# Performance work log

Hardware: AMD Instinct MI355X
Metric: run time of the kernel (lower is better)

The kernel has to match this reference:

```python
import jax, jax.numpy as jnp
import numpy as np

N_NODES = 100000
N_EDGES = 3200000
IN_DIM = 256
HID = 128
OUT = 2
BN_EPS = 1e-5


def setup_inputs() -> dict:
    key = jax.random.key(0)
    ks = jax.random.split(key, 4)
    x = jax.random.normal(ks[0], (N_NODES, IN_DIM), dtype=jnp.float32)
    edge_index = jax.random.randint(ks[1], (2, N_EDGES), 0, N_NODES, dtype=jnp.int64)
    # Glorot-ish scaled weights
    W1 = jax.random.normal(ks[2], (IN_DIM, HID), dtype=jnp.float32) * (1.0 / np.sqrt(IN_DIM))
    W2 = jax.random.normal(ks[3], (HID, OUT), dtype=jnp.float32) * (1.0 / np.sqrt(HID))
    return {
        "x": x,
        "edge_index": edge_index,
        "feature_importance": jnp.ones((IN_DIM,), jnp.float32),
        "W1": W1,
        "b1": jnp.zeros((HID,), jnp.float32),
        "W2": W2,
        "b2": jnp.zeros((OUT,), jnp.float32),
        "gamma": jnp.ones((HID,), jnp.float32),
        "beta": jnp.zeros((HID,), jnp.float32),
    }


def _gcn_conv(x, row, col, norm, W, b, n_nodes):
    # PyG GCNConv: linear transform then D^-1/2 (A+I) D^-1/2 aggregation
    h = x @ W  # [N, d_out]
    msg = h[row] * norm[:, None]  # gather + scale, [E+N, d_out]
    out = jax.ops.segment_sum(msg, col, num_segments=n_nodes)  # scatter-add
    return out + b


def _norm_and_loops(edge_index, n_nodes, dtype):
    loop = jnp.arange(n_nodes, dtype=edge_index.dtype)
    row = jnp.concatenate([edge_index[0], loop])
    col = jnp.concatenate([edge_index[1], loop])
    deg = jax.ops.segment_sum(jnp.ones_like(col, dtype=dtype), col, num_segments=n_nodes)
    dinv = jnp.where(deg > 0, jax.lax.rsqrt(deg), 0.0)
    norm = dinv[row] * dinv[col]
    return row, col, norm


def reference(x, edge_index, feature_importance, W1, b1, W2, b2, gamma, beta):
    n_nodes = x.shape[0]
    row, col, norm = _norm_and_loops(edge_index, n_nodes, x.dtype)
    # sigmoid feature-importance weighting
    xw = x * jax.nn.sigmoid(feature_importance)
    h = _gcn_conv(xw, row, col, norm, W1, b1, n_nodes)
    # BatchNorm1d with batch statistics (training-mode math; dropout omitted = eval)
    mu = jnp.mean(h, axis=0)
    var = jnp.mean((h - mu) ** 2, axis=0)
    h = (h - mu) * jax.lax.rsqrt(var + BN_EPS) * gamma + beta
    h = jax.nn.relu(h)
    out = _gcn_conv(h, row, col, norm, W2, b2, n_nodes)
    return out
```

## Files before the change

kernel.cpp:

```cpp
#include <hip/hip_runtime.h>
#include <hip/hip_bf16.h>

#define N_NODES 100000
#define N_EDGES 3200000
#define IN_DIM 256
#define HID 128
#define BN_EPS 1e-5f
#define SCAN_B 1024
#define NB1 ((N_NODES + SCAN_B - 1) / SCAN_B)

typedef __attribute__((ext_vector_type(8))) short bf16x8;
typedef __attribute__((ext_vector_type(4))) float f32x4;

__device__ __forceinline__ ushort f2bf(float f) {
    unsigned u = __float_as_uint(f);
    u += 0x7FFFu + ((u >> 16) & 1u);
    return (ushort)(u >> 16);
}
__device__ __forceinline__ float bflo(unsigned v) { return __uint_as_float(v << 16); }
__device__ __forceinline__ float bfhi(unsigned v) { return __uint_as_float(v & 0xFFFF0000u); }


__global__ void k_deg(const int* __restrict__ col, unsigned* __restrict__ cnt) {
    int i = blockIdx.x * blockDim.x + threadIdx.x;
    if (i < N_EDGES) atomicAdd(&cnt[col[i]], 1u);
}

__global__ void k_prepw(const float* __restrict__ W1, const float* __restrict__ fi,
                        ushort* __restrict__ W1t) {
    int idx = blockIdx.x * blockDim.x + threadIdx.x;
    if (idx < HID * IN_DIM) {
        int n = idx >> 8, k = idx & 255;
        float s = 1.0f / (1.0f + expf(-fi[k]));
        W1t[idx] = f2bf(W1[k * HID + n] * s);
    }
}


__global__ __launch_bounds__(SCAN_B) void k_scan_part(const unsigned* __restrict__ cnt,
                                                      unsigned* __restrict__ rowptr,
                                                      unsigned* __restrict__ blocksum,
                                                      float* __restrict__ dinv) {
    __shared__ unsigned s[SCAN_B];
    int t = threadIdx.x;
    int i = blockIdx.x * SCAN_B + t;
    unsigned v = (i < N_NODES) ? cnt[i] : 0u;
    if (i < N_NODES) dinv[i] = rsqrtf((float)(v + 1u));
    s[t] = v;
    __syncthreads();
#pragma unroll
    for (int off = 1; off < SCAN_B; off <<= 1) {
        unsigned u = (t >= off) ? s[t - off] : 0u;
        __syncthreads();
        s[t] += u;
        __syncthreads();
    }
    if (i < N_NODES) rowptr[i] = s[t] - v;
    if (t == SCAN_B - 1) blocksum[blockIdx.x] = s[t];
}

__global__ __launch_bounds__(128) void k_scan_mid(const unsigned* __restrict__ blocksum,
                                                  unsigned* __restrict__ blockoff) {
    __shared__ unsigned s[128];
    int t = threadIdx.x;
    unsigned v = (t < NB1) ? blocksum[t] : 0u;
    s[t] = v;
    __syncthreads();
#pragma unroll
    for (int off = 1; off < 128; off <<= 1) {
        unsigned u = (t >= off) ? s[t - off] : 0u;
        __syncthreads();
        s[t] += u;
        __syncthreads();
    }
    if (t < NB1) blockoff[t] = s[t] - v;
}

__global__ void k_scan_add(unsigned* __restrict__ rowptr, const unsigned* __restrict__ blockoff) {
    int i = blockIdx.x * blockDim.x + threadIdx.x;
    if (i < N_NODES) rowptr[i] += blockoff[i >> 10];
    if (i == 0) rowptr[N_NODES] = N_EDGES;
}


__global__ void k_bucket(const int* __restrict__ row, const int* __restrict__ col,
                         const unsigned* __restrict__ rowptr, unsigned* __restrict__ fill,
                         int* __restrict__ esrc) {
    int e = blockIdx.x * blockDim.x + threadIdx.x;
    if (e < N_EDGES) {
        int c = col[e];
        unsigned p = rowptr[c] + atomicAdd(&fill[c], 1u);
        esrc[p] = row[e];
    }
}


__global__ __launch_bounds__(256) void k_gemm1(const float* __restrict__ x,
                                               const ushort* __restrict__ W1t,
                                               const float* __restrict__ dinv,
                                               unsigned* __restrict__ hsu) {
    const int t = threadIdx.x;
    const int w = (blockIdx.x << 2) + (t >> 6);
    const int m0 = w << 4;
    if (m0 >= N_NODES) return;
    const int lane = t & 63;
    const int mrow = lane & 15;
    const int quad = lane >> 4;

    const float* xrow = x + (size_t)(m0 + mrow) * IN_DIM + quad * 8;
    const ushort* wrow = W1t + mrow * IN_DIM + quad * 8;

    f32x4 acc[8] = {};
#pragma unroll
    for (int ks = 0; ks < 8; ++ks) {
        float4 xa = *(const float4*)(xrow + ks * 32);
        float4 xb = *(const float4*)(xrow + ks * 32 + 4);
        bf16x8 bfrag;
        bfrag[0] = (short)f2bf(xa.x); bfrag[1] = (short)f2bf(xa.y);
        bfrag[2] = (short)f2bf(xa.z); bfrag[3] = (short)f2bf(xa.w);
        bfrag[4] = (short)f2bf(xb.x); bfrag[5] = (short)f2bf(xb.y);
        bfrag[6] = (short)f2bf(xb.z); bfrag[7] = (short)f2bf(xb.w);
        const ushort* wk = wrow + ks * 32;
#pragma unroll
        for (int nb = 0; nb < 8; ++nb) {
            bf16x8 afrag = *(const bf16x8*)(wk + nb * 16 * IN_DIM);
            acc[nb] = __builtin_amdgcn_mfma_f32_16x16x32_bf16(afrag, bfrag, acc[nb], 0, 0, 0);
        }
    }
    const float d = dinv[m0 + mrow];
    unsigned* orow = hsu + (size_t)(m0 + mrow) * 64;
#pragma unroll
    for (int nb = 0; nb < 8; ++nb) {
        unsigned p0 = (unsigned)f2bf(acc[nb][0] * d) | ((unsigned)f2bf(acc[nb][1] * d) << 16);
        unsigned p1 = (unsigned)f2bf(acc[nb][2] * d) | ((unsigned)f2bf(acc[nb][3] * d) << 16);
        *(uint2*)(orow + nb * 8 + quad * 2) = make_uint2(p0, p1);
    }
}


__global__ __launch_bounds__(256) void k_agg1csr(const int* __restrict__ esrc,
                                                 const unsigned* __restrict__ rowptr,
                                                 const unsigned* __restrict__ hsu,
                                                 const float* __restrict__ dinv,
                                                 const float* __restrict__ b1,
                                                 unsigned* __restrict__ S1u,
                                                 float* __restrict__ stats) {
    const int t = threadIdx.x;
    const int lane = t & 63;
    const int gw = (blockIdx.x * blockDim.x + t) >> 6;
    const int nw = (gridDim.x * blockDim.x) >> 6;
    const int ch = lane * 2;
    const float2 bb = *(const float2*)&b1[ch];
    float s0 = 0.f, s1 = 0.f, q0 = 0.f, q1 = 0.f;

    for (int c = gw; c < N_NODES; c += nw) {
        const unsigned beg = rowptr[c], end = rowptr[c + 1];
        unsigned self = hsu[(size_t)c * 64 + lane];
        float a0 = bflo(self), a1 = bfhi(self);
        unsigned i = beg;
        for (; i + 8 <= end; i += 8) {
#pragma unroll
            for (int u = 0; u < 8; ++u) {
                int r = esrc[i + u];
                unsigned v = hsu[(size_t)r * 64 + lane];
                a0 += bflo(v); a1 += bfhi(v);
            }
        }
        for (; i < end; ++i) {
            int r = esrc[i];
            unsigned v = hsu[(size_t)r * 64 + lane];
            a0 += bflo(v); a1 += bfhi(v);
        }
        float d = dinv[c];
        float v0 = d * a0 + bb.x;
        float v1 = d * a1 + bb.y;
        S1u[(size_t)c * 64 + lane] = (unsigned)f2bf(v0) | ((unsigned)f2bf(v1) << 16);
        s0 += v0; s1 += v1; q0 += v0 * v0; q1 += v1 * v1;
    }

    __shared__ float red[256];
#define RED_ATOMIC(val, idx)                                              \
    red[t] = (val); __syncthreads();                                      \
    if (t < 64) {                                                         \
        float r_ = red[t] + red[t + 64] + red[t + 128] + red[t + 192];    \
        atomicAdd(&stats[idx], r_);                                       \
    } __syncthreads();
    RED_ATOMIC(s0, ch)
    RED_ATOMIC(s1, ch + 1)
    RED_ATOMIC(q0, 128 + ch)
    RED_ATOMIC(q1, 129 + ch)
#undef RED_ATOMIC
}


__global__ void k_bnfin(const float* __restrict__ stats,
                        const float* __restrict__ gamma,
                        const float* __restrict__ beta,
                        float* __restrict__ bnp) {
    int j = threadIdx.x;
    if (j < HID) {
        float mu = stats[j] * (1.0f / N_NODES);
        float var = stats[128 + j] * (1.0f / N_NODES) - mu * mu;
        float rstd = rsqrtf(var + BN_EPS);
        float sc = rstd * gamma[j];
        bnp[j] = sc;
        bnp[128 + j] = beta[j] - mu * sc;
    }
}


__global__ __launch_bounds__(256) void k_gemm2(const unsigned* __restrict__ S1u,
                                               const float* __restrict__ bnp,
                                               const float* __restrict__ W2,
                                               const float* __restrict__ dinv,
                                               float* __restrict__ gs) {
    int wid = (blockIdx.x * blockDim.x + threadIdx.x) >> 6;
    int lane = threadIdx.x & 63;
    int nw = (gridDim.x * blockDim.x) >> 6;
    int k0 = lane * 2;
    float2 sc = *(const float2*)&bnp[k0];
    float2 sh = *(const float2*)&bnp[128 + k0];
    float4 w = *(const float4*)&W2[k0 * 2];
    for (int n = wid; n < N_NODES; n += nw) {
        unsigned hv = S1u[(size_t)n * 64 + lane];
        float v0 = fmaxf(bflo(hv) * sc.x + sh.x, 0.f);
        float v1 = fmaxf(bfhi(hv) * sc.y + sh.y, 0.f);
        float a0 = v0 * w.x + v1 * w.z;
        float a1 = v0 * w.y + v1 * w.w;
#pragma unroll
        for (int off = 32; off; off >>= 1) {
            a0 += __shfl_down(a0, off);
            a1 += __shfl_down(a1, off);
        }
        if (lane == 0) {
            float d = dinv[n];
            *(float2*)&gs[n * 2] = make_float2(a0 * d, a1 * d);
        }
    }
}


__global__ void k_agg2csr(const int* __restrict__ esrc,
                          const unsigned* __restrict__ rowptr,
                          const float* __restrict__ gs,
                          const float* __restrict__ dinv,
                          const float* __restrict__ b2,
                          float* __restrict__ out) {
    int c = blockIdx.x * blockDim.x + threadIdx.x;
    if (c >= N_NODES) return;
    float2 acc = *(const float2*)&gs[c * 2];
    unsigned beg = rowptr[c], end = rowptr[c + 1];
    unsigned i = beg;
    for (; i + 4 <= end; i += 4) {
#pragma unroll
        for (int u = 0; u < 4; ++u) {
            int r = esrc[i + u];
            float2 v = *(const float2*)&gs[r * 2];
            acc.x += v.x; acc.y += v.y;
        }
    }
    for (; i < end; ++i) {
        int r = esrc[i];
        float2 v = *(const float2*)&gs[r * 2];
        acc.x += v.x; acc.y += v.y;
    }
    float d = dinv[c];
    *(float2*)&out[c * 2] = make_float2(d * acc.x + b2[0], d * acc.y + b2[1]);
}


extern "C" void kernel_launch(void* const* d_in, const int* in_sizes, int n_in,
                              void* d_out, int out_size, void* d_ws, size_t ws_size,
                              hipStream_t stream) {
    const float* x     = (const float*)d_in[0];
    const int*   edge  = (const int*)d_in[1];
    const float* fi    = (const float*)d_in[2];
    const float* W1    = (const float*)d_in[3];
    const float* b1    = (const float*)d_in[4];
    const float* W2    = (const float*)d_in[5];
    const float* b2    = (const float*)d_in[6];
    const float* gamma = (const float*)d_in[7];
    const float* beta  = (const float*)d_in[8];
    float* out = (float*)d_out;

    const int* erow = edge;
    const int* ecol = edge + N_EDGES;

    char* ws = (char*)d_ws;
    size_t off = 0;
    auto alloc = [&](size_t bytes) { size_t r = off; off = (off + bytes + 255) & ~(size_t)255; return r; };
    unsigned* hsu   = (unsigned*)(ws + alloc(sizeof(unsigned) * (size_t)N_NODES * 64));
    unsigned* S1u   = (unsigned*)(ws + alloc(sizeof(unsigned) * (size_t)N_NODES * 64));
    int*      esrc  = (int*)(ws + alloc(sizeof(int) * (size_t)N_EDGES));
    float*    gs    = (float*)(ws + alloc(sizeof(float) * N_NODES * 2));
    unsigned* cnt   = (unsigned*)(ws + alloc(sizeof(unsigned) * N_NODES * 2));
    unsigned* fill  = cnt + N_NODES;
    unsigned* rowptr= (unsigned*)(ws + alloc(sizeof(unsigned) * (N_NODES + 1)));
    unsigned* bsum  = (unsigned*)(ws + alloc(sizeof(unsigned) * NB1));
    unsigned* boff  = (unsigned*)(ws + alloc(sizeof(unsigned) * NB1));
    float*    dinv  = (float*)(ws + alloc(sizeof(float) * N_NODES));
    ushort*   W1t   = (ushort*)(ws + alloc(sizeof(ushort) * HID * IN_DIM));
    float*    stats = (float*)(ws + alloc(sizeof(float) * 2 * HID));
    float*    bnp   = (float*)(ws + alloc(sizeof(float) * 2 * HID));
    (void)ws_size; (void)in_sizes; (void)n_in; (void)out_size;

    hipMemsetAsync(cnt, 0, sizeof(unsigned) * N_NODES * 2, stream);
    hipMemsetAsync(stats, 0, sizeof(float) * 2 * HID, stream);

    k_deg<<<(N_EDGES + 255) / 256, 256, 0, stream>>>(ecol, cnt);
    k_prepw<<<(HID * IN_DIM + 255) / 256, 256, 0, stream>>>(W1, fi, W1t);

    k_scan_part<<<NB1, SCAN_B, 0, stream>>>(cnt, rowptr, bsum, dinv);
    k_scan_mid<<<1, 128, 0, stream>>>(bsum, boff);
    k_scan_add<<<(N_NODES + 255) / 256, 256, 0, stream>>>(rowptr, boff);
    k_bucket<<<(N_EDGES + 255) / 256, 256, 0, stream>>>(erow, ecol, rowptr, fill, esrc);

    k_gemm1<<<(N_NODES / 16 + 3) / 4, 256, 0, stream>>>(x, W1t, dinv, hsu);
    k_agg1csr<<<2048, 256, 0, stream>>>(esrc, rowptr, hsu, dinv, b1, S1u, stats);
    k_bnfin<<<1, 128, 0, stream>>>(stats, gamma, beta, bnp);
    k_gemm2<<<2048, 256, 0, stream>>>(S1u, bnp, W2, dinv, gs);
    k_agg2csr<<<(N_NODES + 255) / 256, 256, 0, stream>>>(esrc, rowptr, gs, dinv, b2, out);
}
```

Before: 747.5 us.

## Vectorize edge loads, split accumulators, fold BN finalize into gemm2

The degree and bucketing kernels now handle two edges per thread with int2 loads, halving the thread count. Both CSR aggregation loops split the sum across two accumulator pairs to break the serial add dependency, and agg2 is unrolled by 8. The separate BatchNorm finalize kernel is removed and each gemm2 thread computes scale and shift from stats directly, saving one launch at the cost of redundant per-thread math. Splitting the accumulators changes the order of floating-point summation.

```diff
diff --git a/kernel.cpp b/kernel.cpp
--- a/kernel.cpp
+++ b/kernel.cpp
@@ -23,7 +23,14 @@
 
 __global__ void k_deg(const int* __restrict__ col, unsigned* __restrict__ cnt) {
     int i = blockIdx.x * blockDim.x + threadIdx.x;
-    if (i < N_EDGES) atomicAdd(&cnt[col[i]], 1u);
+    int e = i * 2;
+    if (e + 1 < N_EDGES) {
+        int2 cc = *(const int2*)&col[e];
+        atomicAdd(&cnt[cc.x], 1u);
+        atomicAdd(&cnt[cc.y], 1u);
+    } else if (e < N_EDGES) {
+        atomicAdd(&cnt[col[e]], 1u);
+    }
 }
 
 __global__ void k_prepw(const float* __restrict__ W1, const float* __restrict__ fi,
@@ -86,8 +93,16 @@
 __global__ void k_bucket(const int* __restrict__ row, const int* __restrict__ col,
                          const unsigned* __restrict__ rowptr, unsigned* __restrict__ fill,
                          int* __restrict__ esrc) {
-    int e = blockIdx.x * blockDim.x + threadIdx.x;
-    if (e < N_EDGES) {
+    int i = blockIdx.x * blockDim.x + threadIdx.x;
+    int e = i * 2;
+    if (e + 1 < N_EDGES) {
+        int2 rr = *(const int2*)&row[e];
+        int2 cc = *(const int2*)&col[e];
+        unsigned p0 = rowptr[cc.x] + atomicAdd(&fill[cc.x], 1u);
+        esrc[p0] = rr.x;
+        unsigned p1 = rowptr[cc.y] + atomicAdd(&fill[cc.y], 1u);
+        esrc[p1] = rr.y;
+    } else if (e < N_EDGES) {
         int c = col[e];
         unsigned p = rowptr[c] + atomicAdd(&fill[c], 1u);
         esrc[p] = row[e];
@@ -157,13 +172,15 @@
         const unsigned beg = rowptr[c], end = rowptr[c + 1];
         unsigned self = hsu[(size_t)c * 64 + lane];
         float a0 = bflo(self), a1 = bfhi(self);
+        float e0 = 0.f, e1 = 0.f;
         unsigned i = beg;
         for (; i + 8 <= end; i += 8) {
 #pragma unroll
             for (int u = 0; u < 8; ++u) {
                 int r = esrc[i + u];
                 unsigned v = hsu[(size_t)r * 64 + lane];
-                a0 += bflo(v); a1 += bfhi(v);
+                if (u & 1) { e0 += bflo(v); e1 += bfhi(v); }
+                else       { a0 += bflo(v); a1 += bfhi(v); }
             }
         }
         for (; i < end; ++i) {
@@ -171,6 +188,7 @@
             unsigned v = hsu[(size_t)r * 64 + lane];
             a0 += bflo(v); a1 += bfhi(v);
         }
+        a0 += e0; a1 += e1;
         float d = dinv[c];
         float v0 = d * a0 + bb.x;
         float v1 = d * a1 + bb.y;
@@ -193,24 +211,10 @@
 }
 
 
-__global__ void k_bnfin(const float* __restrict__ stats,
-                        const float* __restrict__ gamma,
-                        const float* __restrict__ beta,
-                        float* __restrict__ bnp) {
-    int j = threadIdx.x;
-    if (j < HID) {
-        float mu = stats[j] * (1.0f / N_NODES);
-        float var = stats[128 + j] * (1.0f / N_NODES) - mu * mu;
-        float rstd = rsqrtf(var + BN_EPS);
-        float sc = rstd * gamma[j];
-        bnp[j] = sc;
-        bnp[128 + j] = beta[j] - mu * sc;
-    }
-}
-
-
 __global__ __launch_bounds__(256) void k_gemm2(const unsigned* __restrict__ S1u,
-                                               const float* __restrict__ bnp,
+                                               const float* __restrict__ stats,
+                                               const float* __restrict__ gamma,
+                                               const float* __restrict__ beta,
                                                const float* __restrict__ W2,
                                                const float* __restrict__ dinv,
                                                float* __restrict__ gs) {
@@ -218,13 +222,19 @@
     int lane = threadIdx.x & 63;
     int nw = (gridDim.x * blockDim.x) >> 6;
     int k0 = lane * 2;
-    float2 sc = *(const float2*)&bnp[k0];
-    float2 sh = *(const float2*)&bnp[128 + k0];
+    const float inv = 1.0f / (float)N_NODES;
+    float mu0 = stats[k0] * inv, mu1 = stats[k0 + 1] * inv;
+    float va0 = stats[128 + k0] * inv - mu0 * mu0;
+    float va1 = stats[129 + k0] * inv - mu1 * mu1;
+    float sc0 = rsqrtf(va0 + BN_EPS) * gamma[k0];
+    float sc1 = rsqrtf(va1 + BN_EPS) * gamma[k0 + 1];
+    float sh0 = beta[k0] - mu0 * sc0;
+    float sh1 = beta[k0 + 1] - mu1 * sc1;
     float4 w = *(const float4*)&W2[k0 * 2];
     for (int n = wid; n < N_NODES; n += nw) {
         unsigned hv = S1u[(size_t)n * 64 + lane];
-        float v0 = fmaxf(bflo(hv) * sc.x + sh.x, 0.f);
-        float v1 = fmaxf(bfhi(hv) * sc.y + sh.y, 0.f);
+        float v0 = fmaxf(bflo(hv) * sc0 + sh0, 0.f);
+        float v1 = fmaxf(bfhi(hv) * sc1 + sh1, 0.f);
         float a0 = v0 * w.x + v1 * w.z;
         float a1 = v0 * w.y + v1 * w.w;
 #pragma unroll
@@ -240,23 +250,25 @@
 }
 
 
-__global__ void k_agg2csr(const int* __restrict__ esrc,
-                          const unsigned* __restrict__ rowptr,
-                          const float* __restrict__ gs,
-                          const float* __restrict__ dinv,
-                          const float* __restrict__ b2,
-                          float* __restrict__ out) {
+__global__ __launch_bounds__(256) void k_agg2csr(const int* __restrict__ esrc,
+                                                 const unsigned* __restrict__ rowptr,
+                                                 const float* __restrict__ gs,
+                                                 const float* __restrict__ dinv,
+                                                 const float* __restrict__ b2,
+                                                 float* __restrict__ out) {
     int c = blockIdx.x * blockDim.x + threadIdx.x;
     if (c >= N_NODES) return;
     float2 acc = *(const float2*)&gs[c * 2];
+    float2 acc2 = make_float2(0.f, 0.f);
     unsigned beg = rowptr[c], end = rowptr[c + 1];
     unsigned i = beg;
-    for (; i + 4 <= end; i += 4) {
-#pragma unroll
-        for (int u = 0; u < 4; ++u) {
+    for (; i + 8 <= end; i += 8) {
+#pragma unroll
+        for (int u = 0; u < 8; ++u) {
             int r = esrc[i + u];
             float2 v = *(const float2*)&gs[r * 2];
-            acc.x += v.x; acc.y += v.y;
+            if (u & 1) { acc2.x += v.x; acc2.y += v.y; }
+            else       { acc.x += v.x; acc.y += v.y; }
         }
     }
     for (; i < end; ++i) {
@@ -264,6 +276,7 @@
         float2 v = *(const float2*)&gs[r * 2];
         acc.x += v.x; acc.y += v.y;
     }
+    acc.x += acc2.x; acc.y += acc2.y;
     float d = dinv[c];
     *(float2*)&out[c * 2] = make_float2(d * acc.x + b2[0], d * acc.y + b2[1]);
 }
@@ -301,23 +314,21 @@
     float*    dinv  = (float*)(ws + alloc(sizeof(float) * N_NODES));
     ushort*   W1t   = (ushort*)(ws + alloc(sizeof(ushort) * HID * IN_DIM));
     float*    stats = (float*)(ws + alloc(sizeof(float) * 2 * HID));
-    float*    bnp   = (float*)(ws + alloc(sizeof(float) * 2 * HID));
     (void)ws_size; (void)in_sizes; (void)n_in; (void)out_size;
 
     hipMemsetAsync(cnt, 0, sizeof(unsigned) * N_NODES * 2, stream);
     hipMemsetAsync(stats, 0, sizeof(float) * 2 * HID, stream);
 
-    k_deg<<<(N_EDGES + 255) / 256, 256, 0, stream>>>(ecol, cnt);
+    k_deg<<<(N_EDGES / 2 + 255) / 256, 256, 0, stream>>>(ecol, cnt);
     k_prepw<<<(HID * IN_DIM + 255) / 256, 256, 0, stream>>>(W1, fi, W1t);
 
     k_scan_part<<<NB1, SCAN_B, 0, stream>>>(cnt, rowptr, bsum, dinv);
     k_scan_mid<<<1, 128, 0, stream>>>(bsum, boff);
     k_scan_add<<<(N_NODES + 255) / 256, 256, 0, stream>>>(rowptr, boff);
-    k_bucket<<<(N_EDGES + 255) / 256, 256, 0, stream>>>(erow, ecol, rowptr, fill, esrc);
+    k_bucket<<<(N_EDGES / 2 + 255) / 256, 256, 0, stream>>>(erow, ecol, rowptr, fill, esrc);
 
     k_gemm1<<<(N_NODES / 16 + 3) / 4, 256, 0, stream>>>(x, W1t, dinv, hsu);
     k_agg1csr<<<2048, 256, 0, stream>>>(esrc, rowptr, hsu, dinv, b1, S1u, stats);
-    k_bnfin<<<1, 128, 0, stream>>>(stats, gamma, beta, bnp);
-    k_gemm2<<<2048, 256, 0, stream>>>(S1u, bnp, W2, dinv, gs);
+    k_gemm2<<<2048, 256, 0, stream>>>(S1u, stats, gamma, beta, W2, dinv, gs);
     k_agg2csr<<<(N_NODES + 255) / 256, 256, 0, stream>>>(esrc, rowptr, gs, dinv, b2, out);
 }
```

New measurement: 744.9 us. No clear change (-0.3%).
